# Optimization experiments

Measured on AMD Instinct MI355X. Metric: run time of the kernel, lower is better.

## Reference

```python
import jax, jax.numpy as jnp
import numpy as np

RES = 14
KEY_DIM = 32
NUM_HEADS = 12
ATTN_RATIO = 4
DIM = 384
VAL_ATTN_DIM = ATTN_RATIO * KEY_DIM * NUM_HEADS  # 1536
QKV_DIM = VAL_ATTN_DIM + 2 * KEY_DIM * NUM_HEADS  # 2304
BN_EPS = 1e-5


def _bias_idxs():
    # torch.meshgrid default is 'ij'
    gy, gx = jnp.meshgrid(jnp.arange(RES), jnp.arange(RES), indexing='ij')
    pos = jnp.stack([gy.reshape(-1), gx.reshape(-1)])           # [2, N]
    rel = jnp.abs(pos[:, :, None] - pos[:, None, :])            # [2, N, N]
    return rel[0] * RES + rel[1]                                # [N, N] int


def _linear_bn(x, w, gamma, beta, mean, var):
    # bias-free Linear (torch weight layout [out,in]) + BatchNorm1d (eval)
    y = x @ w.T
    inv = gamma / jnp.sqrt(var + BN_EPS)
    return y * inv + (beta - mean * inv)


def setup_inputs() -> dict:
    key = jax.random.key(0)
    ks = jax.random.split(key, 12)
    B, N = 128, RES * RES
    f = jax.random.normal
    return {
        'x': f(ks[0], (B, N, DIM), jnp.float32),
        'qkv_w': f(ks[1], (QKV_DIM, DIM), jnp.float32) * 0.02,
        'qkv_gamma': f(ks[2], (QKV_DIM,), jnp.float32) * 0.1 + 1.0,
        'qkv_beta': f(ks[3], (QKV_DIM,), jnp.float32) * 0.1,
        'qkv_mean': f(ks[4], (QKV_DIM,), jnp.float32) * 0.1,
        'qkv_var': jax.random.uniform(ks[5], (QKV_DIM,), jnp.float32, 0.5, 1.5),
        'attn_biases': f(ks[6], (NUM_HEADS, RES * RES), jnp.float32) * 0.1,
        'proj_w': f(ks[7], (DIM, VAL_ATTN_DIM), jnp.float32) * 0.02,
        'proj_gamma': f(ks[8], (DIM,), jnp.float32) * 0.1 + 1.0,
        'proj_beta': f(ks[9], (DIM,), jnp.float32) * 0.1,
        'proj_mean': f(ks[10], (DIM,), jnp.float32) * 0.1,
        'proj_var': jax.random.uniform(ks[11], (DIM,), jnp.float32, 0.5, 1.5),
    }


def reference(x, qkv_w, qkv_gamma, qkv_beta, qkv_mean, qkv_var,
              attn_biases, proj_w, proj_gamma, proj_beta, proj_mean, proj_var):
    B, N, _ = x.shape
    scale = KEY_DIM ** -0.5
    qkv = _linear_bn(x, qkv_w, qkv_gamma, qkv_beta, qkv_mean, qkv_var)
    qkv = qkv.reshape(B, N, NUM_HEADS, -1)
    q = qkv[..., :KEY_DIM]                       # [B,N,H,dk]
    k = qkv[..., KEY_DIM:2 * KEY_DIM]            # [B,N,H,dk]
    v = qkv[..., 2 * KEY_DIM:]                   # [B,N,H,dv]
    bias = attn_biases[:, _bias_idxs()]          # [H,N,N]
    attn = jnp.einsum('bnhd,bmhd->bhnm', q, k) * scale + bias[None]
    attn = jax.nn.softmax(attn, axis=-1)
    out = jnp.einsum('bhnm,bmhd->bnhd', attn, v).reshape(B, N, VAL_ATTN_DIM)
    out = jax.nn.silu(out)
    return _linear_bn(out, proj_w, proj_gamma, proj_beta, proj_mean, proj_var)
```

## Files before the change

### kernel.cpp

```cpp
#include <hip/hip_runtime.h>
#include <cstdint>

#define NQ 196
#define DIMX 384
#define QKVD 2304
#define VAD 1536
#define NHD 12
#define MTOT 25088

#define KSTR 40
#define VSTR 232
#define VTS 224
#define BTS 208
#define TSTR 140

typedef unsigned int u32;
typedef unsigned short u16;
typedef __bf16 bf16_t;
typedef bf16_t bf16x8 __attribute__((ext_vector_type(8)));
typedef float f32x4 __attribute__((ext_vector_type(4)));

__device__ inline u16 f2b(float f) {
  u32 u = __float_as_uint(f);
  u32 r = (u + 0x7fffu + ((u >> 16) & 1u)) >> 16;
  return (u16)r;
}
__device__ inline float b2f(u16 u) { return __uint_as_float(((u32)u) << 16); }
__device__ inline int iabs(int v) { return v < 0 ? -v : v; }

__device__ inline void gld_lds16(const void* g, void* l) {
  __builtin_amdgcn_global_load_lds((__attribute__((address_space(1))) void*)g,
                                   (__attribute__((address_space(3))) void*)l,
                                   16, 0, 0);
}


__global__ void cvt_kernel(const float* __restrict__ in, u16* __restrict__ out, int n4) {
  int i = blockIdx.x * 256 + threadIdx.x;
  if (i >= n4) return;
  float4 v = ((const float4*)in)[i];
  ushort4 o;
  o.x = f2b(v.x); o.y = f2b(v.y); o.z = f2b(v.z); o.w = f2b(v.w);
  ((ushort4*)out)[i] = o;
}

__global__ void cvt_wqkv(const float* __restrict__ in, u16* __restrict__ out) {
  int i = blockIdx.x * 256 + threadIdx.x;
  if (i >= QKVD * DIMX / 4) return;
  const int newc = i / (DIMX / 4);
  const int kc = (i - newc * (DIMX / 4)) * 4;
  int oldc;
  if (newc < 384)      { int h = newc >> 5;              oldc = h * 192 + (newc & 31); }
  else if (newc < 768) { int t = newc - 384; int h = t >> 5; oldc = h * 192 + 32 + (t & 31); }
  else                 { int t = newc - 768; int h = t >> 7; oldc = h * 192 + 64 + (t & 127); }
  float4 v = *(const float4*)(in + (size_t)oldc * DIMX + kc);
  ushort4 o;
  o.x = f2b(v.x); o.y = f2b(v.y); o.z = f2b(v.z); o.w = f2b(v.w);
  *(ushort4*)(out + (size_t)newc * DIMX + kc) = o;
}

__global__ void bn_tab(const float* __restrict__ g, const float* __restrict__ be,
                       const float* __restrict__ mn, const float* __restrict__ vr,
                       float* __restrict__ inv, float* __restrict__ off, int n) {
  int i = blockIdx.x * 256 + threadIdx.x;
  if (i >= n) return;
  float iv = g[i] * rsqrtf(vr[i] + 1e-5f);
  inv[i] = iv;
  off[i] = be[i] - mn[i] * iv;
}

__global__ void bn_tab_qkv(const float* __restrict__ g, const float* __restrict__ be,
                           const float* __restrict__ mn, const float* __restrict__ vr,
                           float* __restrict__ inv, float* __restrict__ off) {
  int i = blockIdx.x * 256 + threadIdx.x;
  if (i >= QKVD) return;
  const int h = i / 192, r = i - h * 192;
  const int newc = (r < 32) ? h * 32 + r
                 : (r < 64) ? 384 + h * 32 + (r - 32)
                            : 768 + h * 128 + (r - 64);
  float iv = g[i] * rsqrtf(vr[i] + 1e-5f);
  inv[newc] = iv;
  off[newc] = be[i] - mn[i] * iv;
}

__global__ void bias_expand(const float* __restrict__ biases, float* __restrict__ bt) {
  int i = blockIdx.x * 256 + threadIdx.x;
  if (i >= NHD * BTS * BTS) return;
  const int h = i / (BTS * BTS), r = i - h * BTS * BTS;
  const int m = r / BTS, n = r - m * BTS;
  float v = -1e30f;
  if (m < NQ && n < NQ) {
    const int ym = m / 14, xm = m - ym * 14;
    const int yn = n / 14, xn = n - yn * 14;
    v = biases[h * NQ + iabs(yn - ym) * 14 + iabs(xn - xm)];
  }
  bt[i] = v;
}

__global__ void pad_vt(u16* __restrict__ Vt) {
  int i = blockIdx.x * 256 + threadIdx.x;
  if (i >= 128 * NHD * 128 * 14) return;
  const int row = i / 14, c = i - row * 14;
  *(u32*)(Vt + (size_t)row * VTS + NQ + c * 2) = 0u;
}


template <int MODE>
__global__ __launch_bounds__(256) void gemm_bt(
    const u16* __restrict__ A, const u16* __restrict__ B, int K,
    const float* __restrict__ inv, const float* __restrict__ off,
    u16* __restrict__ Qb, u16* __restrict__ Kb, u16* __restrict__ Vt,
    float* __restrict__ out) {
  constexpr int LDSU = (MODE == 0) ? 128 * TSTR : 8192;
  __shared__ __align__(16) u16 lds[LDSU];
  u16* As = lds;
  u16* Bs = lds + 4096;
  const int tid = threadIdx.x;
  const int wid = tid >> 6, lane = tid & 63;
  const int wm = wid & 1, wn = wid >> 1;
  const int fr = lane & 15, fk = (lane >> 4) << 3;
  const u16* Ab = A + (size_t)(blockIdx.y * 128) * K;
  const u16* Bb = B + (size_t)(blockIdx.x * 128) * K;
  const int c0 = (wid << 6) | lane;
  const int r0 = c0 >> 2, kc0 = (c0 & 3) << 3;
  const int c1 = c0 + 256;
  const int r1 = c1 >> 2, kc1 = (c1 & 3) << 3;

  f32x4 acc[4][4] = {};

  for (int k0 = 0; k0 < K; k0 += 32) {
    gld_lds16(Ab + (size_t)r0 * K + (k0 + kc0), &As[wid << 9]);
    gld_lds16(Ab + (size_t)r1 * K + (k0 + kc1), &As[2048 + (wid << 9)]);
    gld_lds16(Bb + (size_t)r0 * K + (k0 + kc0), &Bs[wid << 9]);
    gld_lds16(Bb + (size_t)r1 * K + (k0 + kc1), &Bs[2048 + (wid << 9)]);
    __syncthreads();
    bf16x8 av[4], bv[4];
#pragma unroll
    for (int t = 0; t < 4; t++)
      av[t] = *(const bf16x8*)&As[(wm * 64 + t * 16 + fr) * 32 + fk];
#pragma unroll
    for (int t = 0; t < 4; t++)
      bv[t] = *(const bf16x8*)&Bs[(wn * 64 + t * 16 + fr) * 32 + fk];
#pragma unroll
    for (int mt = 0; mt < 4; mt++)
#pragma unroll
      for (int nt = 0; nt < 4; nt++)
        acc[mt][nt] = __builtin_amdgcn_mfma_f32_16x16x32_bf16(av[mt], bv[nt], acc[mt][nt], 0, 0, 0);
    __syncthreads();
  }

  const int lrow0 = wm * 64 + ((lane >> 4) << 2);
  const int lcol0 = wn * 64 + fr;

  if (MODE == 0) {
    const int bx = blockIdx.x, by = blockIdx.y;
    const bool isV = bx >= 6;
#pragma unroll
    for (int nt = 0; nt < 4; nt++) {
      const int lc = lcol0 + nt * 16;
      const int gc = bx * 128 + lc;
      const float iv = inv[gc], of = off[gc];
#pragma unroll
      for (int mt = 0; mt < 4; mt++)
#pragma unroll
        for (int rg = 0; rg < 4; rg++) {
          const int lr = lrow0 + mt * 16 + rg;
          const u16 us = f2b(acc[mt][nt][rg] * iv + of);
          if (isV) lds[lc * TSTR + lr] = us;
          else     lds[lr * TSTR + lc] = us;
        }
    }
    __syncthreads();
    if (!isV) {
      u16* dstB = (bx < 3) ? Qb : Kb;
      const int h0 = (bx < 3 ? bx : bx - 3) * 4;
#pragma unroll
      for (int it = 0; it < 8; it++) {
        const int idx = it * 256 + tid;
        const int ch = idx & 3, hl = (idx >> 2) & 3, row = idx >> 4;
        const int rowg = by * 128 + row;
        const int b = rowg / 196, n = rowg - b * 196;
        const size_t bh = (size_t)(b * NHD + h0 + hl);
        const u16* src = &lds[row * TSTR + hl * 32 + ch * 8];
        uint2 a0 = *(const uint2*)src;
        uint2 a1 = *(const uint2*)(src + 4);
        *(uint4*)(dstB + (bh * NQ + n) * 32 + ch * 8) = make_uint4(a0.x, a0.y, a1.x, a1.y);
      }
    } else {
      const int h = bx - 6;
#pragma unroll
      for (int it = 0; it < 16; it++) {
        const int idx = it * 256 + tid;
        const int nk = idx & 31, col = idx >> 5;
        const int rowg = by * 128 + nk * 4;
        const int b = rowg / 196, n = rowg - b * 196;
        uint2 v = *(const uint2*)&lds[col * TSTR + nk * 4];
        *(uint2*)(Vt + ((size_t)(b * NHD + h) * 128 + col) * VTS + n) = v;
      }
    }
  } else {
    const int colb = blockIdx.x * 128 + lcol0;
    const int rowb = blockIdx.y * 128 + lrow0;
#pragma unroll
    for (int nt = 0; nt < 4; nt++) {
      const int col = colb + nt * 16;
      const float iv = inv[col], of = off[col];
#pragma unroll
      for (int mt = 0; mt < 4; mt++)
#pragma unroll
        for (int rg = 0; rg < 4; rg++) {
          const int row = rowb + mt * 16 + rg;
          out[(size_t)row * DIMX + col] = acc[mt][nt][rg] * iv + of;
        }
    }
  }
}


__global__ __launch_bounds__(512) void attn_kernel(
    const u16* __restrict__ Qg, const u16* __restrict__ Kg,
    const u16* __restrict__ Vtg, const float* __restrict__ biasT,
    u16* __restrict__ AO) {
  __shared__ __align__(16) u16 Ks[208 * KSTR];
  __shared__ __align__(16) u16 Vs[128 * VSTR];
  __shared__ __align__(16) u16 Ps[8][16 * VSTR];

  const int tid = threadIdx.x, wid = tid >> 6, lane = tid & 63;
  const int fr = lane & 15, fj = lane >> 4, fk = fj << 3;
  const int bh = blockIdx.x, b = bh / NHD, h = bh - b * NHD;
  const float scale = 0.17677669529663687f;

  for (int i = tid; i < NQ * 4; i += 512) {
    const int m = i >> 2, kc = (i & 3) << 3;
    *(uint4*)&Ks[m * KSTR + kc] = *(const uint4*)(Kg + ((size_t)bh * NQ + m) * 32 + kc);
  }
  if (tid < 48) {
    const int m = 196 + (tid >> 2), kc = (tid & 3) << 3;
    *(uint4*)&Ks[m * KSTR + kc] = make_uint4(0u, 0u, 0u, 0u);
  }
  {
    const u16* Vb = Vtg + (size_t)bh * 128 * VTS;
    for (int i = tid; i < 128 * 28; i += 512) {
      const int d = i / 28, c = i - d * 28;
      *(uint4*)&Vs[d * VSTR + c * 8] = *(const uint4*)(Vb + (size_t)d * VTS + c * 8);
    }
  }
  {
    const int row = lane >> 2, c = 208 + (lane & 3) * 4;
    *(uint2*)&Ps[wid][row * VSTR + c] = make_uint2(0u, 0u);
  }
  __syncthreads();

  const float* bT = biasT + (size_t)h * BTS * BTS;

  for (int rt = wid; rt < 13; rt += 8) {
    int qrow = rt * 16 + fr; qrow = qrow > 195 ? 195 : qrow;
    const bf16x8 qf = *(const bf16x8*)(Qg + ((size_t)bh * NQ + qrow) * 32 + fk);

    f32x4 s[13];
#pragma unroll
    for (int t = 0; t < 13; t++) {
      const bf16x8 kf = *(const bf16x8*)&Ks[(t * 16 + fr) * KSTR + fk];
      f32x4 z = {0.f, 0.f, 0.f, 0.f};
      s[t] = __builtin_amdgcn_mfma_f32_16x16x32_bf16(qf, kf, z, 0, 0, 0);
    }

    const int n0 = rt * 16 + (fj << 2);
    const float* bRow = bT + n0;
#pragma unroll
    for (int t = 0; t < 13; t++) {
      const float4 bv = *(const float4*)(bRow + (size_t)(t * 16 + fr) * BTS);
      s[t][0] = s[t][0] * scale + bv.x;
      s[t][1] = s[t][1] * scale + bv.y;
      s[t][2] = s[t][2] * scale + bv.z;
      s[t][3] = s[t][3] * scale + bv.w;
    }

    float rinv[4];
#pragma unroll
    for (int rg = 0; rg < 4; rg++) {
      float mx = s[0][rg];
#pragma unroll
      for (int t = 1; t < 13; t++) mx = fmaxf(mx, s[t][rg]);
      mx = fmaxf(mx, __shfl_xor(mx, 1));
      mx = fmaxf(mx, __shfl_xor(mx, 2));
      mx = fmaxf(mx, __shfl_xor(mx, 4));
      mx = fmaxf(mx, __shfl_xor(mx, 8));
      float ls = 0.f;
#pragma unroll
      for (int t = 0; t < 13; t++) {
        const float e = __expf(s[t][rg] - mx);
        s[t][rg] = e;
        ls += e;
      }
      ls += __shfl_xor(ls, 1);
      ls += __shfl_xor(ls, 2);
      ls += __shfl_xor(ls, 4);
      ls += __shfl_xor(ls, 8);
      rinv[rg] = 1.f / ls;
    }
#pragma unroll
    for (int t = 0; t < 13; t++)
#pragma unroll
      for (int rg = 0; rg < 4; rg++)
        Ps[wid][(fj * 4 + rg) * VSTR + t * 16 + fr] = f2b(s[t][rg]);
    __threadfence_block();

    f32x4 o[8] = {};
#pragma unroll
    for (int kc = 0; kc < 7; kc++) {
      const bf16x8 pf = *(const bf16x8*)&Ps[wid][fr * VSTR + kc * 32 + fk];
#pragma unroll
      for (int dt = 0; dt < 8; dt++) {
        const bf16x8 vf = *(const bf16x8*)&Vs[(dt * 16 + fr) * VSTR + kc * 32 + fk];
        o[dt] = __builtin_amdgcn_mfma_f32_16x16x32_bf16(pf, vf, o[dt], 0, 0, 0);
      }
    }
#pragma unroll
    for (int rg = 0; rg < 4; rg++) {
      const int n = rt * 16 + fj * 4 + rg;
      if (n < NQ) {
        const float rv = rinv[rg];
#pragma unroll
        for (int dt = 0; dt < 8; dt++) {
          float x = o[dt][rg] * rv;
          x = x / (1.f + __expf(-x));
          AO[((size_t)(b * NQ + n)) * VAD + h * 128 + dt * 16 + fr] = f2b(x);
        }
      }
    }
    __threadfence_block();
  }
}


extern "C" void kernel_launch(void* const* d_in, const int* in_sizes, int n_in,
                              void* d_out, int out_size, void* d_ws, size_t ws_size,
                              hipStream_t stream) {
  const float* x          = (const float*)d_in[0];
  const float* qkv_w      = (const float*)d_in[1];
  const float* qkv_gamma  = (const float*)d_in[2];
  const float* qkv_beta   = (const float*)d_in[3];
  const float* qkv_mean   = (const float*)d_in[4];
  const float* qkv_var    = (const float*)d_in[5];
  const float* attn_bias  = (const float*)d_in[6];
  const float* proj_w     = (const float*)d_in[7];
  const float* proj_gamma = (const float*)d_in[8];
  const float* proj_beta  = (const float*)d_in[9];
  const float* proj_mean  = (const float*)d_in[10];
  const float* proj_var   = (const float*)d_in[11];

  const size_t szXB    = (size_t)MTOT * DIMX * 2;
  const size_t szQKVW  = (size_t)QKVD * DIMX * 2;
  const size_t szPROJW = (size_t)DIMX * VAD * 2;
  const size_t szQK    = (size_t)128 * NHD * NQ * 32 * 2;
  const size_t szV     = (size_t)128 * NHD * 128 * VTS * 2;
  const size_t szBT    = (size_t)NHD * BTS * BTS * 4;
  const size_t szAO    = (size_t)MTOT * VAD * 2;
  const size_t szX     = (szXB + szQKVW > szAO) ? (szXB + szQKVW) : szAO;

  char* w = (char*)d_ws;
  u16* projwb = (u16*)w; w += szPROJW;
  float* inv1 = (float*)w; w += QKVD * 4;
  float* off1 = (float*)w; w += QKVD * 4;
  float* inv2 = (float*)w; w += DIMX * 4;
  float* off2 = (float*)w; w += DIMX * 4;
  float* biasT = (float*)w; w += szBT;
  u16* Qb = (u16*)w; w += szQK;
  u16* Kb = (u16*)w; w += szQK;
  u16* Vt = (u16*)w; w += szV;
  char* regionX = w; w += szX;
  u16* xb    = (u16*)regionX;
  u16* qkvwb = (u16*)(regionX + szXB);
  u16* AO    = (u16*)regionX;

  if ((size_t)(w - (char*)d_ws) > ws_size) return;

  cvt_kernel<<<MTOT * DIMX / 4 / 256, 256, 0, stream>>>(x, xb, MTOT * DIMX / 4);
  cvt_wqkv<<<(QKVD * DIMX / 4 + 255) / 256, 256, 0, stream>>>(qkv_w, qkvwb);
  cvt_kernel<<<DIMX * VAD / 4 / 256, 256, 0, stream>>>(proj_w, projwb, DIMX * VAD / 4);
  bn_tab_qkv<<<(QKVD + 255) / 256, 256, 0, stream>>>(qkv_gamma, qkv_beta, qkv_mean, qkv_var, inv1, off1);
  bn_tab<<<(DIMX + 255) / 256, 256, 0, stream>>>(proj_gamma, proj_beta, proj_mean, proj_var, inv2, off2, DIMX);
  bias_expand<<<(NHD * BTS * BTS + 255) / 256, 256, 0, stream>>>(attn_bias, biasT);
  pad_vt<<<(128 * NHD * 128 * 14 + 255) / 256, 256, 0, stream>>>(Vt);

  gemm_bt<0><<<dim3(QKVD / 128, MTOT / 128), 256, 0, stream>>>(
      xb, qkvwb, DIMX, inv1, off1, Qb, Kb, Vt, nullptr);
  attn_kernel<<<128 * NHD, 512, 0, stream>>>(Qb, Kb, Vt, biasT, AO);
  gemm_bt<1><<<dim3(DIMX / 128, MTOT / 128), 256, 0, stream>>>(
      AO, projwb, VAD, inv2, off2, nullptr, nullptr, nullptr, (float*)d_out);
}
```

Baseline: 395.2 us.

## Keep softmax probabilities in registers by transposing QK^T and permuting V layout

The QK^T MFMA operands are swapped so each lane holds a full query row's scores, which makes the softmax reduction lane-local plus two cross-group shuffles. The probabilities are normalised and packed straight into MFMA A-operand registers instead of going through a per-wave LDS staging buffer. To make that register layout match the PV MFMA's K ordering, the QKV epilogue writes V^T with a permuted key order within each 32-key chunk. The change also adds an occupancy hint to launch bounds, and it depends on the permutation exactly matching the register packing.

```diff
diff --git a/kernel.cpp b/kernel.cpp
--- a/kernel.cpp
+++ b/kernel.cpp
@@ -195,7 +195,9 @@
         const int rowg = by * 128 + nk * 4;
         const int b = rowg / 196, n = rowg - b * 196;
         uint2 v = *(const uint2*)&lds[col * TSTR + nk * 4];
-        *(uint2*)(Vt + ((size_t)(b * NHD + h) * 128 + col) * VTS + n) = v;
+        const int kcB = n >> 5, r = (n >> 2) & 7;
+        const int np = (kcB << 5) + ((((r & 3) << 1) + (r >> 2)) << 2);
+        *(uint2*)(Vt + ((size_t)(b * NHD + h) * 128 + col) * VTS + np) = v;
       }
     }
   } else {
@@ -217,13 +219,12 @@
 }
 
 
-__global__ __launch_bounds__(512) void attn_kernel(
+__global__ __launch_bounds__(512, 4) void attn_kernel(
     const u16* __restrict__ Qg, const u16* __restrict__ Kg,
     const u16* __restrict__ Vtg, const float* __restrict__ biasT,
     u16* __restrict__ AO) {
   __shared__ __align__(16) u16 Ks[208 * KSTR];
   __shared__ __align__(16) u16 Vs[128 * VSTR];
-  __shared__ __align__(16) u16 Ps[8][16 * VSTR];
 
   const int tid = threadIdx.x, wid = tid >> 6, lane = tid & 63;
   const int fr = lane & 15, fj = lane >> 4, fk = fj << 3;
@@ -245,10 +246,6 @@
       *(uint4*)&Vs[d * VSTR + c * 8] = *(const uint4*)(Vb + (size_t)d * VTS + c * 8);
     }
   }
-  {
-    const int row = lane >> 2, c = 208 + (lane & 3) * 4;
-    *(uint2*)&Ps[wid][row * VSTR + c] = make_uint2(0u, 0u);
-  }
   __syncthreads();
 
   const float* bT = biasT + (size_t)h * BTS * BTS;
@@ -262,74 +259,79 @@
     for (int t = 0; t < 13; t++) {
       const bf16x8 kf = *(const bf16x8*)&Ks[(t * 16 + fr) * KSTR + fk];
       f32x4 z = {0.f, 0.f, 0.f, 0.f};
-      s[t] = __builtin_amdgcn_mfma_f32_16x16x32_bf16(qf, kf, z, 0, 0, 0);
-    }
-
-    const int n0 = rt * 16 + (fj << 2);
-    const float* bRow = bT + n0;
+      s[t] = __builtin_amdgcn_mfma_f32_16x16x32_bf16(kf, qf, z, 0, 0, 0);
+    }
+
+    const int q = rt * 16 + fr;
+    const float* bRow = bT + (size_t)q * BTS + (fj << 2);
 #pragma unroll
     for (int t = 0; t < 13; t++) {
-      const float4 bv = *(const float4*)(bRow + (size_t)(t * 16 + fr) * BTS);
+      const float4 bv = *(const float4*)(bRow + t * 16);
       s[t][0] = s[t][0] * scale + bv.x;
       s[t][1] = s[t][1] * scale + bv.y;
       s[t][2] = s[t][2] * scale + bv.z;
       s[t][3] = s[t][3] * scale + bv.w;
     }
 
-    float rinv[4];
-#pragma unroll
-    for (int rg = 0; rg < 4; rg++) {
-      float mx = s[0][rg];
-#pragma unroll
-      for (int t = 1; t < 13; t++) mx = fmaxf(mx, s[t][rg]);
-      mx = fmaxf(mx, __shfl_xor(mx, 1));
-      mx = fmaxf(mx, __shfl_xor(mx, 2));
-      mx = fmaxf(mx, __shfl_xor(mx, 4));
-      mx = fmaxf(mx, __shfl_xor(mx, 8));
-      float ls = 0.f;
-#pragma unroll
-      for (int t = 0; t < 13; t++) {
+    float mx = fmaxf(fmaxf(s[0][0], s[0][1]), fmaxf(s[0][2], s[0][3]));
+#pragma unroll
+    for (int t = 1; t < 13; t++)
+      mx = fmaxf(mx, fmaxf(fmaxf(s[t][0], s[t][1]), fmaxf(s[t][2], s[t][3])));
+    mx = fmaxf(mx, __shfl_xor(mx, 16));
+    mx = fmaxf(mx, __shfl_xor(mx, 32));
+    float ls = 0.f;
+#pragma unroll
+    for (int t = 0; t < 13; t++)
+#pragma unroll
+      for (int rg = 0; rg < 4; rg++) {
         const float e = __expf(s[t][rg] - mx);
         s[t][rg] = e;
         ls += e;
       }
-      ls += __shfl_xor(ls, 1);
-      ls += __shfl_xor(ls, 2);
-      ls += __shfl_xor(ls, 4);
-      ls += __shfl_xor(ls, 8);
-      rinv[rg] = 1.f / ls;
-    }
-#pragma unroll
-    for (int t = 0; t < 13; t++)
-#pragma unroll
-      for (int rg = 0; rg < 4; rg++)
-        Ps[wid][(fj * 4 + rg) * VSTR + t * 16 + fr] = f2b(s[t][rg]);
-    __threadfence_block();
+    ls += __shfl_xor(ls, 16);
+    ls += __shfl_xor(ls, 32);
+    const float rinv = 1.f / ls;
+#pragma unroll
+    for (int t = 0; t < 13; t++) {
+      s[t][0] *= rinv; s[t][1] *= rinv; s[t][2] *= rinv; s[t][3] *= rinv;
+    }
 
     f32x4 o[8] = {};
 #pragma unroll
     for (int kc = 0; kc < 7; kc++) {
-      const bf16x8 pf = *(const bf16x8*)&Ps[wid][fr * VSTR + kc * 32 + fk];
+      bf16x8 pf;
+      pf[0] = (bf16_t)s[2 * kc][0];
+      pf[1] = (bf16_t)s[2 * kc][1];
+      pf[2] = (bf16_t)s[2 * kc][2];
+      pf[3] = (bf16_t)s[2 * kc][3];
+      if (kc < 6) {
+        pf[4] = (bf16_t)s[2 * kc + 1][0];
+        pf[5] = (bf16_t)s[2 * kc + 1][1];
+        pf[6] = (bf16_t)s[2 * kc + 1][2];
+        pf[7] = (bf16_t)s[2 * kc + 1][3];
+      } else {
+        pf[4] = (bf16_t)0.f; pf[5] = (bf16_t)0.f;
+        pf[6] = (bf16_t)0.f; pf[7] = (bf16_t)0.f;
+      }
 #pragma unroll
       for (int dt = 0; dt < 8; dt++) {
         const bf16x8 vf = *(const bf16x8*)&Vs[(dt * 16 + fr) * VSTR + kc * 32 + fk];
         o[dt] = __builtin_amdgcn_mfma_f32_16x16x32_bf16(pf, vf, o[dt], 0, 0, 0);
       }
     }
+
 #pragma unroll
     for (int rg = 0; rg < 4; rg++) {
       const int n = rt * 16 + fj * 4 + rg;
-      if (n < NQ) {
-        const float rv = rinv[rg];
+      if (n < 196) {
 #pragma unroll
         for (int dt = 0; dt < 8; dt++) {
-          float x = o[dt][rg] * rv;
+          float x = o[dt][rg];
           x = x / (1.f + __expf(-x));
           AO[((size_t)(b * NQ + n)) * VAD + h * 128 + dt * 16 + fr] = f2b(x);
         }
       }
     }
-    __threadfence_block();
   }
 }
 
```

Result: slower. 812.2 us (+105.5%).
